# Optimization experiments

Hardware: AMD Instinct MI355X
Metric: run time of the kernel (lower is better)

Reference implementation:

```python
import jax, jax.numpy as jnp
import numpy as np
from jax import lax

B, CIN, H, W = 64, 3, 64, 64
HID = 128          # hidden_dim == embedding_dim
K = 1024           # num_embeddings
BETA = 0.25        # commitment cost


def _conv(x, w, b, stride):
    # torch Conv2d, padding=0, NCHW / OIHW weights
    y = lax.conv_general_dilated(x, w, (stride, stride), 'VALID',
                                 dimension_numbers=('NCHW', 'OIHW', 'NCHW'))
    return y + b[None, :, None, None]


def _conv_transpose(x, w, b, stride):
    # torch ConvTranspose2d, padding=0; w is [Cin, Cout, kh, kw] (torch layout)
    kh, kw = w.shape[2], w.shape[3]
    w2 = jnp.flip(w, (2, 3)).transpose(1, 0, 2, 3)  # -> OIHW, spatially flipped
    y = lax.conv_general_dilated(x, w2, (1, 1),
                                 [(kh - 1, kh - 1), (kw - 1, kw - 1)],
                                 lhs_dilation=(stride, stride),
                                 dimension_numbers=('NCHW', 'OIHW', 'NCHW'))
    return y + b[None, :, None, None]


def setup_inputs() -> dict:
    key = jax.random.key(0)
    ks = jax.random.split(key, 10)
    s = 0.05
    return {
        'x':      jax.random.normal(ks[0], (B, CIN, H, W), jnp.float32),
        'enc_w1': jax.random.normal(ks[1], (HID, CIN, 4, 4), jnp.float32) * s,
        'enc_b1': jnp.zeros((HID,), jnp.float32),
        'enc_w2': jax.random.normal(ks[2], (HID, HID, 2, 2), jnp.float32) * s,
        'enc_b2': jnp.zeros((HID,), jnp.float32),
        'codebook': jax.random.uniform(ks[3], (K, HID), jnp.float32,
                                       minval=-1.0 / K, maxval=1.0 / K),
        'dec_w1': jax.random.normal(ks[4], (HID, HID, 2, 2), jnp.float32) * s,
        'dec_b1': jnp.zeros((HID,), jnp.float32),
        'dec_w2': jax.random.normal(ks[5], (HID, CIN, 4, 4), jnp.float32) * s,
        'dec_b2': jnp.zeros((CIN,), jnp.float32),
    }


def reference(x, enc_w1, enc_b1, enc_w2, enc_b2, codebook,
              dec_w1, dec_b1, dec_w2, dec_b2):
    # ---- encoder ----
    z = jax.nn.relu(_conv(x, enc_w1, enc_b1, 2))
    z = jax.nn.relu(_conv(z, enc_w2, enc_b2, 1))   # [B, HID, 30, 30]

    # ---- vector quantizer (faithful to torch reshape semantics) ----
    D = HID
    flat = z.reshape(-1, D)                        # [N, D], C-order rows
    # squared euclidean distances (argmin identical to torch.cdist argmin)
    d2 = (jnp.sum(flat * flat, axis=1, keepdims=True)
          - 2.0 * flat @ codebook.T
          + jnp.sum(codebook * codebook, axis=1)[None, :])  # [N, K]
    idx = jnp.argmin(d2, axis=1)                   # [N]
    quantized = codebook[idx].reshape(z.shape)

    e_latent = jnp.mean((lax.stop_gradient(quantized) - z) ** 2)
    q_latent = jnp.mean((quantized - lax.stop_gradient(z)) ** 2)
    loss = q_latent + BETA * e_latent

    q_st = z + lax.stop_gradient(quantized - z)    # straight-through

    n = flat.shape[0]
    avg_probs = jnp.zeros((K,), z.dtype).at[idx].add(1.0) / n
    perplexity = jnp.exp(-jnp.sum(avg_probs * jnp.log(avg_probs + 1e-10)))

    # ---- decoder ----
    y = jax.nn.relu(_conv_transpose(q_st, dec_w1, dec_b1, 1))
    x_recon = _conv_transpose(y, dec_w2, dec_b2, 2)  # [B, 3, 64, 64]
    return x_recon, loss, perplexity
```

## Files before the change

### kernel.cpp

```cpp
#include <hip/hip_runtime.h>

#define B_    64
#define CIN_  3
#define HW_   64
#define HID_  128
#define K_    1024
#define H1_   31
#define H2_   30
#define NROWS_ 57600
#define NELEM_ 7372800

typedef __bf16 bf16_t;
typedef __attribute__((ext_vector_type(8))) __bf16 bf16x8;
typedef __attribute__((ext_vector_type(4))) float f32x4;

__global__ __launch_bounds__(256) void wprep_k(const float* __restrict__ ew1,
    const float* __restrict__ ew2, const float* __restrict__ dw1,
    const float* __restrict__ dw2, const float* __restrict__ cb,
    bf16_t* __restrict__ wc1, bf16_t* __restrict__ wc2,
    bf16_t* __restrict__ wd1, bf16_t* __restrict__ wt2,
    bf16_t* __restrict__ cbb, float* __restrict__ cnorm,
    unsigned* __restrict__ hist, float* __restrict__ sse) {
  int id = blockIdx.x * 256 + threadIdx.x;
  int t = id >> 14, co = (id >> 7) & 127, ci = id & 127;
  wc2[id] = (bf16_t)ew2[(co * 128 + ci) * 4 + t];
  wd1[id] = (bf16_t)dw1[(ci * 128 + co) * 4 + (3 - t)];
  if (id < 8192) {
    int n = id >> 9, k = id & 511;
    int tap = k >> 7, c = k & 127;
    if (n < 12) {
      int nco = n >> 2, ph = (n >> 1) & 1, pw = n & 1;
      int off = (tap >> 1) * 8 + (tap & 1) * 2;
      wt2[id] = (bf16_t)dw2[c * 48 + nco * 16 + ph * 4 + pw + off];
    } else {
      wt2[id] = (bf16_t)0.f;
    }
    int c1 = id >> 6, k1 = id & 63;
    wc1[id] = (bf16_t)(k1 < 48 ? ew1[c1 * 48 + k1] : 0.f);
  }
  if (id < K_) {
    float s0 = 0.f;
    for (int d = 0; d < HID_; d += 4) {
      float4 v = *(const float4*)&cb[id * HID_ + d];
      bf16_t tt[4] = {(bf16_t)v.x, (bf16_t)v.y, (bf16_t)v.z, (bf16_t)v.w};
      *(ushort4*)&((ushort*)cbb)[id * HID_ + d] = *(ushort4*)tt;
      float f0 = (float)tt[0], f1 = (float)tt[1];
      float f2 = (float)tt[2], f3 = (float)tt[3];
      s0 += f0 * f0 + f1 * f1 + f2 * f2 + f3 * f3;
    }
    cnorm[id] = s0;
    hist[id] = 0u;
  }
  if (id == 0) *sse = 0.f;
}

__global__ __launch_bounds__(256, 2) void conv1m_k(const float* __restrict__ x,
    const bf16_t* __restrict__ wc1, const float* __restrict__ bias,
    ushort* __restrict__ z1t) {
  __shared__ __align__(16) bf16_t as_[64 * 72];
  __shared__ __align__(16) bf16_t bs_[128 * 72];
  int b = blockIdx.x >> 4, rt = blockIdx.x & 15;
  int tid = threadIdx.x, wv = tid >> 6, ln = tid & 63;
  const float* xb = x + (size_t)b * 12288;
  #pragma unroll
  for (int it = 0; it < 16; ++it) {
    int e = it * 256 + tid;
    int p = e >> 6, k = e & 63;
    float v = 0.f;
    if (k < 48) {
      int ci = k >> 4, kh = (k >> 2) & 3, kw = k & 3;
      int row = 2 * rt + (p >> 5); if (row > 30) row = 30;
      int col = p & 31;            if (col > 30) col = 30;
      v = xb[ci * 4096 + (2 * row + kh) * 64 + 2 * col + kw];
    }
    as_[p * 72 + k] = (bf16_t)v;
  }
  {
    const float4* wg = (const float4*)wc1;
    #pragma unroll
    for (int it = 0; it < 4; ++it) {
      int fi = it * 256 + tid;
      int co = fi >> 3, k8 = fi & 7;
      *(float4*)&bs_[co * 72 + k8 * 8] = wg[fi];
    }
  }
  __syncthreads();
  int q = ln >> 4, l = ln & 15;
  f32x4 acc8[8];
  #pragma unroll
  for (int c = 0; c < 8; ++c) acc8[c] = (f32x4){0.f, 0.f, 0.f, 0.f};
  bf16x8 af[2];
  #pragma unroll
  for (int kk = 0; kk < 2; ++kk)
    af[kk] = *(const bf16x8*)&as_[(wv * 16 + l) * 72 + kk * 32 + q * 8];
  #pragma unroll
  for (int cot = 0; cot < 8; ++cot) {
    #pragma unroll
    for (int kk = 0; kk < 2; ++kk) {
      bf16x8 bf = *(const bf16x8*)&bs_[(cot * 16 + l) * 72 + kk * 32 + q * 8];
      acc8[cot] = __builtin_amdgcn_mfma_f32_16x16x32_bf16(af[kk], bf,
                                                          acc8[cot], 0, 0, 0);
    }
  }
  #pragma unroll
  for (int cot = 0; cot < 8; ++cot) {
    int co = cot * 16 + l;
    float bv = bias[co];
    #pragma unroll
    for (int r = 0; r < 4; ++r) {
      int pos = wv * 16 + q * 4 + r;
      int prow = 2 * rt + (pos >> 5), pcol = pos & 31;
      if (prow < 31 && pcol < 31) {
        float v = fmaxf(acc8[cot][r] + bv, 0.f);
        bf16_t h = (bf16_t)v;
        z1t[((size_t)(b * 1024 + prow * 32 + pcol)) * 128 + co] = *(ushort*)&h;
      }
    }
  }
}

__global__ __launch_bounds__(256, 2) void conv2m_k(const bf16_t* __restrict__ z1t,
    const bf16_t* __restrict__ wc2, const float* __restrict__ bias,
    float* __restrict__ z, ushort* __restrict__ zbuf) {
  __shared__ __align__(16) bf16_t as_[98 * 136];
  __shared__ __align__(16) bf16_t bs_[128 * 136];
  int blk = blockIdx.x;
  int b = blk / 15, rt = blk % 15;
  int tid = threadIdx.x, wv = tid >> 6, ln = tid & 63;
  const float4* src = (const float4*)(z1t + ((size_t)b * 1024 + rt * 64) * 128);
  #pragma unroll
  for (int s = 0; s < 7; ++s) {
    int f = s * 256 + tid;
    if (f < 1568) {
      int lp = f >> 4, c16 = f & 15;
      *(float4*)&as_[lp * 136 + c16 * 8] = src[f];
    }
  }
  int m = wv * 16 + (ln & 15), q = ln >> 4;
  f32x4 acc8[8];
  #pragma unroll
  for (int c = 0; c < 8; ++c) acc8[c] = (f32x4){0.f, 0.f, 0.f, 0.f};
  const float4* w4 = (const float4*)wc2;
  #pragma unroll
  for (int t = 0; t < 4; ++t) {
    __syncthreads();
    #pragma unroll
    for (int s = 0; s < 8; ++s) {
      int f = s * 256 + tid;
      int co = f >> 4, c16 = f & 15;
      *(float4*)&bs_[co * 136 + c16 * 8] = w4[t * 2048 + f];
    }
    __syncthreads();
    int off = (t >> 1) * 32 + (t & 1);
    bf16x8 af[4];
    #pragma unroll
    for (int kk = 0; kk < 4; ++kk)
      af[kk] = *(const bf16x8*)&as_[(m + off) * 136 + kk * 32 + q * 8];
    #pragma unroll
    for (int cot = 0; cot < 8; ++cot) {
      #pragma unroll
      for (int kk = 0; kk < 4; ++kk) {
        bf16x8 bf = *(const bf16x8*)&bs_[(cot * 16 + (ln & 15)) * 136 +
                                         kk * 32 + q * 8];
        acc8[cot] = __builtin_amdgcn_mfma_f32_16x16x32_bf16(af[kk], bf,
                                                            acc8[cot], 0, 0, 0);
      }
    }
  }
  #pragma unroll
  for (int cot = 0; cot < 8; ++cot) {
    int co = cot * 16 + (ln & 15);
    float bv = bias[co];
    #pragma unroll
    for (int r = 0; r < 4; ++r) {
      int mo = wv * 16 + q * 4 + r;
      int ocol = mo & 31;
      if (ocol < 30) {
        int orow = rt * 2 + (mo >> 5);
        float v = fmaxf(acc8[cot][r] + bv, 0.f);
        size_t idx = (size_t)(b * HID_ + co) * 900 + orow * 30 + ocol;
        z[idx] = v;
        bf16_t h = (bf16_t)v;
        zbuf[idx] = *(ushort*)&h;
      }
    }
  }
}

__global__ __launch_bounds__(256) void zero_k(float4* __restrict__ p, int n4) {
  int i = blockIdx.x * 256 + threadIdx.x;
  if (i < n4) p[i] = make_float4(0.f, 0.f, 0.f, 0.f);
}

__global__ __launch_bounds__(256, 2) void vq1_k(const bf16_t* __restrict__ zb,
    const bf16_t* __restrict__ cbb, const float* __restrict__ cnorm,
    int* __restrict__ idxArr, unsigned* __restrict__ hist) {
  __shared__ __align__(16) bf16_t zs[64 * 136];
  __shared__ __align__(16) bf16_t cbs[128 * 136];
  __shared__ unsigned long long red[64 * 16];
  __shared__ float cns[K_];
  int n0 = blockIdx.x * 64;
  int tid = threadIdx.x;
  int wv = tid >> 6, ln = tid & 63;
  {
    const float4* zg4 = (const float4*)(zb + (size_t)n0 * HID_);
    #pragma unroll
    for (int s = 0; s < 4; ++s) {
      int f = s * 256 + tid;
      int row = f >> 4, seg = f & 15;
      *(float4*)&zs[row * 136 + seg * 8] = zg4[f];
    }
    ((float4*)cns)[tid] = ((const float4*)cnorm)[tid];
  }
  __syncthreads();
  bf16x8 afr[4];
  #pragma unroll
  for (int kk = 0; kk < 4; ++kk)
    afr[kk] = *(const bf16x8*)&zs[(wv * 16 + (ln & 15)) * 136 + kk * 32 +
                                  (ln >> 4) * 8];
  unsigned long long best[4] = {~0ull, ~0ull, ~0ull, ~0ull};
  const float4* cg4 = (const float4*)cbb;
  for (int c0 = 0; c0 < K_; c0 += 128) {
    __syncthreads();
    #pragma unroll
    for (int s = 0; s < 8; ++s) {
      int f = s * 256 + tid;
      int code = f >> 4, seg = f & 15;
      *(float4*)&cbs[code * 136 + seg * 8] = cg4[(c0 + code) * 16 + seg];
    }
    __syncthreads();
    #pragma unroll 2
    for (int t = 0; t < 8; ++t) {
      f32x4 acc = {0.f, 0.f, 0.f, 0.f};
      #pragma unroll
      for (int kk = 0; kk < 4; ++kk) {
        bf16x8 bfr = *(const bf16x8*)&cbs[(t * 16 + (ln & 15)) * 136 +
                                          kk * 32 + (ln >> 4) * 8];
        acc = __builtin_amdgcn_mfma_f32_16x16x32_bf16(afr[kk], bfr, acc,
                                                      0, 0, 0);
      }
      int code = c0 + t * 16 + (ln & 15);
      float cn = cns[code];
      #pragma unroll
      for (int r = 0; r < 4; ++r) {
        float dist = cn - 2.f * acc[r];
        unsigned u = __float_as_uint(dist);
        u = (u & 0x80000000u) ? ~u : (u | 0x80000000u);
        unsigned long long p = ((unsigned long long)u << 32) | (unsigned)code;
        if (p < best[r]) best[r] = p;
      }
    }
  }
  __syncthreads();
  #pragma unroll
  for (int r = 0; r < 4; ++r)
    red[(wv * 16 + (ln >> 4) * 4 + r) * 16 + (ln & 15)] = best[r];
  __syncthreads();
  if (tid < 64) {
    unsigned long long b = ~0ull;
    #pragma unroll
    for (int c = 0; c < 16; ++c) {
      unsigned long long p = red[tid * 16 + c];
      if (p < b) b = p;
    }
    int bi = (int)(b & 0xffffffffu);
    idxArr[n0 + tid] = bi;
    atomicAdd(&hist[bi], 1u);
  }
}

__global__ __launch_bounds__(256) void tq_k(const bf16_t* __restrict__ cbb,
    const int* __restrict__ idxArr, ushort* __restrict__ qt) {
  __shared__ ushort t[60 * 128];
  int b = blockIdx.x / 15, st = blockIdx.x % 15;
  int tid = threadIdx.x;
  int s0 = st * 60;
  #pragma unroll
  for (int it = 0; it < 8; ++it) {
    int task = it * 256 + tid;
    if (task < 1920) {
      int sc = task >> 7, c = task & 127;
      int f = b * 115200 + c * 900 + s0 + sc * 4;
      int n = f >> 7, d = f & 127;
      int k = idxArr[n];
      ushort4 v = *(const ushort4*)((const ushort*)cbb + k * 128 + d);
      t[(sc * 4 + 0) * 128 + c] = v.x;
      t[(sc * 4 + 1) * 128 + c] = v.y;
      t[(sc * 4 + 2) * 128 + c] = v.z;
      t[(sc * 4 + 3) * 128 + c] = v.w;
    }
  }
  __syncthreads();
  #pragma unroll
  for (int it = 0; it < 4; ++it) {
    int task = it * 256 + tid;
    if (task < 960) {
      int sl = task >> 4, c16 = task & 15;
      int s = s0 + sl;
      int h = s / 30, w = s - h * 30;
      int p = (h + 1) * 32 + (w + 1);
      *(uint4*)&qt[((size_t)(b * 1024 + p)) * 128 + c16 * 8] =
          *(uint4*)&t[sl * 128 + c16 * 8];
    }
  }
}

__global__ __launch_bounds__(256) void sse_k(const float4* __restrict__ z4,
    const float* __restrict__ cb, const int* __restrict__ idxArr,
    float* __restrict__ sse) {
  int base = blockIdx.x * 2048 + threadIdx.x;
  float se = 0.f;
  #pragma unroll
  for (int it = 0; it < 8; ++it) {
    int i = base + it * 256;
    int f = i * 4;
    int n = f >> 7, d = f & 127;
    int k = idxArr[n];
    float4 zv = z4[i];
    float4 cv = *(const float4*)&cb[k * 128 + d];
    float dx = cv.x - zv.x, dy = cv.y - zv.y;
    float dz = cv.z - zv.z, dw = cv.w - zv.w;
    se += dx * dx + dy * dy + dz * dz + dw * dw;
  }
  #pragma unroll
  for (int o = 32; o > 0; o >>= 1) se += __shfl_down(se, o, 64);
  __shared__ float red[4];
  if ((threadIdx.x & 63) == 0) red[threadIdx.x >> 6] = se;
  __syncthreads();
  if (threadIdx.x == 0)
    atomicAdd(sse, red[0] + red[1] + red[2] + red[3]);
}

__global__ __launch_bounds__(256, 2) void convt1m_k(const bf16_t* __restrict__ qt,
    const bf16_t* __restrict__ wd1, const float* __restrict__ bias,
    ushort* __restrict__ yt) {
  __shared__ __align__(16) bf16_t as_[98 * 136];
  __shared__ __align__(16) bf16_t bs_[128 * 136];
  int blk = blockIdx.x;
  int b = blk >> 4, rt = blk & 15;
  int tid = threadIdx.x, wv = tid >> 6, ln = tid & 63;
  const float4* src = (const float4*)(qt + (size_t)b * 1024 * 128);
  #pragma unroll
  for (int s = 0; s < 7; ++s) {
    int f = s * 256 + tid;
    if (f < 1568) {
      int lp = f >> 4, c16 = f & 15;
      int gr = rt * 64 + lp;
      if (gr > 1023) gr = 1023;
      *(float4*)&as_[lp * 136 + c16 * 8] = src[gr * 16 + c16];
    }
  }
  int m = wv * 16 + (ln & 15), q = ln >> 4;
  f32x4 acc8[8];
  #pragma unroll
  for (int c = 0; c < 8; ++c) acc8[c] = (f32x4){0.f, 0.f, 0.f, 0.f};
  const float4* w4 = (const float4*)wd1;
  #pragma unroll
  for (int t = 0; t < 4; ++t) {
    __syncthreads();
    #pragma unroll
    for (int s = 0; s < 8; ++s) {
      int f = s * 256 + tid;
      int co = f >> 4, c16 = f & 15;
      *(float4*)&bs_[co * 136 + c16 * 8] = w4[t * 2048 + f];
    }
    __syncthreads();
    int off = (t >> 1) * 32 + (t & 1);
    bf16x8 af[4];
    #pragma unroll
    for (int kk = 0; kk < 4; ++kk)
      af[kk] = *(const bf16x8*)&as_[(m + off) * 136 + kk * 32 + q * 8];
    #pragma unroll
    for (int cot = 0; cot < 8; ++cot) {
      #pragma unroll
      for (int kk = 0; kk < 4; ++kk) {
        bf16x8 bf = *(const bf16x8*)&bs_[(cot * 16 + (ln & 15)) * 136 +
                                         kk * 32 + q * 8];
        acc8[cot] = __builtin_amdgcn_mfma_f32_16x16x32_bf16(af[kk], bf,
                                                            acc8[cot], 0, 0, 0);
      }
    }
  }
  #pragma unroll
  for (int cot = 0; cot < 8; ++cot) {
    int co = cot * 16 + (ln & 15);
    float bv = bias[co];
    #pragma unroll
    for (int r = 0; r < 4; ++r) {
      int mo = wv * 16 + q * 4 + r;
      int orow = rt * 2 + (mo >> 5), ocol = mo & 31;
      if (orow < 31 && ocol < 31) {
        float v = fmaxf(acc8[cot][r] + bv, 0.f);
        bf16_t h = (bf16_t)v;
        yt[((size_t)b * 1156 + (orow + 1) * 34 + (ocol + 1)) * 128 + co] =
            *(ushort*)&h;
      }
    }
  }
}

__global__ __launch_bounds__(256, 2) void convt2m_k(const bf16_t* __restrict__ yt,
    const bf16_t* __restrict__ wt2, const float* __restrict__ bias,
    float* __restrict__ out) {
  __shared__ __align__(16) bf16_t as_[128 * 136];
  int b = blockIdx.x >> 4, rt = blockIdx.x & 15;
  int tid = threadIdx.x, wv = tid >> 6, ln = tid & 63;
  const float4* src = (const float4*)(yt + ((size_t)b * 1156 + rt * 68) * 128);
  #pragma unroll
  for (int s = 0; s < 8; ++s) {
    int f = s * 256 + tid;
    int lp = f >> 4, c16 = f & 15;
    *(float4*)&as_[lp * 136 + c16 * 8] = src[f];
  }
  __syncthreads();
  int mloc = wv * 16 + (ln & 15), q = ln >> 4;
  int qh = mloc >> 5, qw = mloc & 31;
  int base = (qh + 1) * 34 + qw + 1;
  f32x4 acc = {0.f, 0.f, 0.f, 0.f};
  #pragma unroll
  for (int kc = 0; kc < 16; ++kc) {
    int tap = kc >> 2;
    int toff = (tap & 1) + (tap >> 1) * 34;
    bf16x8 af = *(const bf16x8*)&as_[(base - toff) * 136 +
                                     (kc & 3) * 32 + q * 8];
    bf16x8 bf = *(const bf16x8*)&wt2[(size_t)(ln & 15) * 512 + kc * 32 + q * 8];
    acc = __builtin_amdgcn_mfma_f32_16x16x32_bf16(af, bf, acc, 0, 0, 0);
  }
  __syncthreads();
  float* bb = (float*)as_;
  #pragma unroll
  for (int r = 0; r < 4; ++r)
    bb[(wv * 16 + q * 4 + r) * 16 + (ln & 15)] = acc[r];
  __syncthreads();
  if (tid < 192) {
    int row_id = tid >> 4;
    int co = row_id >> 2, ohoff = row_id & 3;
    int qhl = ohoff >> 1, ph = ohoff & 1;
    float bv = bias[co];
    int ow0 = (tid & 15) * 4;
    float tmp[4];
    #pragma unroll
    for (int e = 0; e < 4; ++e) {
      int ow = ow0 + e;
      tmp[e] = bb[(qhl * 32 + (ow >> 1)) * 16 + co * 4 + ph * 2 + (ow & 1)]
               + bv;
    }
    *(float4*)&out[((size_t)(b * 3 + co)) * 4096 + (rt * 4 + ohoff) * 64 + ow0]
        = *(float4*)tmp;
  }
}

__global__ __launch_bounds__(256) void fin_k(const unsigned* __restrict__ hist,
    const float* __restrict__ sse, float* __restrict__ out) {
  __shared__ float red[256];
  float e = 0.f;
  for (int k = threadIdx.x; k < K_; k += 256) {
    float p = (float)hist[k] * (1.0f / (float)NROWS_);
    e += p * logf(p + 1e-10f);
  }
  red[threadIdx.x] = e;
  __syncthreads();
  #pragma unroll
  for (int t = 128; t > 0; t >>= 1) {
    if (threadIdx.x < t) red[threadIdx.x] += red[threadIdx.x + t];
    __syncthreads();
  }
  if (threadIdx.x == 0) {
    out[786432] = 1.25f * (*sse) * (1.0f / (float)NELEM_);
    out[786433] = expf(-red[0]);
  }
}

extern "C" void kernel_launch(void* const* d_in, const int* in_sizes, int n_in,
                              void* d_out, int out_size, void* d_ws,
                              size_t ws_size, hipStream_t stream) {
  (void)in_sizes; (void)n_in; (void)out_size; (void)ws_size;
  const float* x   = (const float*)d_in[0];
  const float* ew1 = (const float*)d_in[1];
  const float* eb1 = (const float*)d_in[2];
  const float* ew2 = (const float*)d_in[3];
  const float* eb2 = (const float*)d_in[4];
  const float* cb  = (const float*)d_in[5];
  const float* dw1 = (const float*)d_in[6];
  const float* db1 = (const float*)d_in[7];
  const float* dw2 = (const float*)d_in[8];
  const float* db2 = (const float*)d_in[9];
  float* out = (float*)d_out;
  char* ws = (char*)d_ws;

  ushort*   yt    = (ushort*)(ws);
  float*    z     = (float*)(ws + 35684352);
  bf16_t*   z1t   = (bf16_t*)(ws + 65175552);
  bf16_t*   qt    = (bf16_t*)(ws + 65175552);
  ushort*   zbuf  = (ushort*)(ws + 81985536);
  bf16_t*   cbb   = (bf16_t*)(ws + 96731136);
  bf16_t*   wc2   = (bf16_t*)(ws + 96993280);
  bf16_t*   wd1   = (bf16_t*)(ws + 97124352);
  int*      idxArr= (int*)(ws + 97255424);
  unsigned* hist  = (unsigned*)(ws + 97485824);
  float*    cnorm = (float*)(ws + 97489920);
  float*    sse   = (float*)(ws + 97494016);
  bf16_t*   wt2   = (bf16_t*)(ws + 97497088);
  bf16_t*   wc1   = (bf16_t*)(ws + 97513472);

  wprep_k<<<dim3(256), dim3(256), 0, stream>>>(ew1, ew2, dw1, dw2, cb,
                                               wc1, wc2, wd1, wt2,
                                               cbb, cnorm, hist, sse);
  conv1m_k<<<dim3(1024), dim3(256), 0, stream>>>(x, wc1, eb1, (ushort*)z1t);
  conv2m_k<<<dim3(960), dim3(256), 0, stream>>>(z1t, wc2, eb2, z, zbuf);
  vq1_k<<<dim3(900), dim3(256), 0, stream>>>((const bf16_t*)zbuf, cbb, cnorm,
                                             idxArr, hist);
  zero_k<<<dim3(4624), dim3(256), 0, stream>>>((float4*)yt, 1183744);
  zero_k<<<dim3(4104), dim3(256), 0, stream>>>((float4*)qt, 1050624);
  tq_k<<<dim3(960), dim3(256), 0, stream>>>(cbb, idxArr, (ushort*)qt);
  sse_k<<<dim3(900), dim3(256), 0, stream>>>((const float4*)z, cb, idxArr,
                                             sse);
  convt1m_k<<<dim3(1024), dim3(256), 0, stream>>>(qt, wd1, db1, yt);
  convt2m_k<<<dim3(1024), dim3(256), 0, stream>>>((const bf16_t*)yt, wt2, db2,
                                                  out);
  fin_k<<<dim3(1), dim3(256), 0, stream>>>(hist, sse, out);
}
```

Measured before the change: 270.8 us.

## Zero only padding halos, fuse gather/SSE kernels, fold finalize into decoder

Removes the two full-buffer zeroing passes over the padded qt and yt activation buffers. Only the halo border cells are now zeroed: qt's borders in extra blocks of a new fused gather+SSE kernel, and yt's borders inside convt1m before its interior writes. The codebook gather/transpose and the SSE reduction are merged into one launch by splitting on block index, and the perplexity/loss finalize is folded into block 0 of convt2m. This cuts tens of MB of memory writes and several kernel launches. In exchange the border-index logic must exactly match the padding layout, and block 0 of convt2m does extra work.

```diff
diff --git a/kernel.cpp b/kernel.cpp
--- a/kernel.cpp
+++ b/kernel.cpp
@@ -187,11 +187,6 @@
   }
 }
 
-__global__ __launch_bounds__(256) void zero_k(float4* __restrict__ p, int n4) {
-  int i = blockIdx.x * 256 + threadIdx.x;
-  if (i < n4) p[i] = make_float4(0.f, 0.f, 0.f, 0.f);
-}
-
 __global__ __launch_bounds__(256, 2) void vq1_k(const bf16_t* __restrict__ zb,
     const bf16_t* __restrict__ cbb, const float* __restrict__ cnorm,
     int* __restrict__ idxArr, unsigned* __restrict__ hist) {
@@ -269,66 +264,82 @@
   }
 }
 
-__global__ __launch_bounds__(256) void tq_k(const bf16_t* __restrict__ cbb,
-    const int* __restrict__ idxArr, ushort* __restrict__ qt) {
+__global__ __launch_bounds__(256) void tqsse_k(const float4* __restrict__ z4,
+    const float* __restrict__ cb, const bf16_t* __restrict__ cbb,
+    const int* __restrict__ idxArr, ushort* __restrict__ qt,
+    float* __restrict__ sse) {
   __shared__ ushort t[60 * 128];
-  int b = blockIdx.x / 15, st = blockIdx.x % 15;
-  int tid = threadIdx.x;
-  int s0 = st * 60;
-  #pragma unroll
-  for (int it = 0; it < 8; ++it) {
-    int task = it * 256 + tid;
-    if (task < 1920) {
-      int sc = task >> 7, c = task & 127;
-      int f = b * 115200 + c * 900 + s0 + sc * 4;
+  __shared__ float red4[4];
+  int bid = blockIdx.x, tid = threadIdx.x;
+  if (bid < 900) {
+    int base = bid * 2048 + tid;
+    float se = 0.f;
+    #pragma unroll
+    for (int it = 0; it < 8; ++it) {
+      int i = base + it * 256;
+      int f = i * 4;
       int n = f >> 7, d = f & 127;
       int k = idxArr[n];
-      ushort4 v = *(const ushort4*)((const ushort*)cbb + k * 128 + d);
-      t[(sc * 4 + 0) * 128 + c] = v.x;
-      t[(sc * 4 + 1) * 128 + c] = v.y;
-      t[(sc * 4 + 2) * 128 + c] = v.z;
-      t[(sc * 4 + 3) * 128 + c] = v.w;
-    }
-  }
-  __syncthreads();
-  #pragma unroll
-  for (int it = 0; it < 4; ++it) {
-    int task = it * 256 + tid;
-    if (task < 960) {
-      int sl = task >> 4, c16 = task & 15;
-      int s = s0 + sl;
-      int h = s / 30, w = s - h * 30;
-      int p = (h + 1) * 32 + (w + 1);
-      *(uint4*)&qt[((size_t)(b * 1024 + p)) * 128 + c16 * 8] =
-          *(uint4*)&t[sl * 128 + c16 * 8];
-    }
-  }
-}
-
-__global__ __launch_bounds__(256) void sse_k(const float4* __restrict__ z4,
-    const float* __restrict__ cb, const int* __restrict__ idxArr,
-    float* __restrict__ sse) {
-  int base = blockIdx.x * 2048 + threadIdx.x;
-  float se = 0.f;
-  #pragma unroll
-  for (int it = 0; it < 8; ++it) {
-    int i = base + it * 256;
-    int f = i * 4;
-    int n = f >> 7, d = f & 127;
-    int k = idxArr[n];
-    float4 zv = z4[i];
-    float4 cv = *(const float4*)&cb[k * 128 + d];
-    float dx = cv.x - zv.x, dy = cv.y - zv.y;
-    float dz = cv.z - zv.z, dw = cv.w - zv.w;
-    se += dx * dx + dy * dy + dz * dz + dw * dw;
-  }
-  #pragma unroll
-  for (int o = 32; o > 0; o >>= 1) se += __shfl_down(se, o, 64);
-  __shared__ float red[4];
-  if ((threadIdx.x & 63) == 0) red[threadIdx.x >> 6] = se;
-  __syncthreads();
-  if (threadIdx.x == 0)
-    atomicAdd(sse, red[0] + red[1] + red[2] + red[3]);
+      float4 zv = z4[i];
+      float4 cv = *(const float4*)&cb[k * 128 + d];
+      float dx = cv.x - zv.x, dy = cv.y - zv.y;
+      float dz = cv.z - zv.z, dw = cv.w - zv.w;
+      se += dx * dx + dy * dy + dz * dz + dw * dw;
+    }
+    #pragma unroll
+    for (int o = 32; o > 0; o >>= 1) se += __shfl_down(se, o, 64);
+    if ((tid & 63) == 0) red4[tid >> 6] = se;
+    __syncthreads();
+    if (tid == 0) atomicAdd(sse, red4[0] + red4[1] + red4[2] + red4[3]);
+  } else if (bid < 1860) {
+    int tb = bid - 900;
+    int b = tb / 15, st = tb % 15;
+    int s0 = st * 60;
+    #pragma unroll
+    for (int it = 0; it < 8; ++it) {
+      int task = it * 256 + tid;
+      if (task < 1920) {
+        int sc = task >> 7, c = task & 127;
+        int f = b * 115200 + c * 900 + s0 + sc * 4;
+        int n = f >> 7, d = f & 127;
+        int k = idxArr[n];
+        ushort4 v = *(const ushort4*)((const ushort*)cbb + k * 128 + d);
+        t[(sc * 4 + 0) * 128 + c] = v.x;
+        t[(sc * 4 + 1) * 128 + c] = v.y;
+        t[(sc * 4 + 2) * 128 + c] = v.z;
+        t[(sc * 4 + 3) * 128 + c] = v.w;
+      }
+    }
+    __syncthreads();
+    #pragma unroll
+    for (int it = 0; it < 4; ++it) {
+      int task = it * 256 + tid;
+      if (task < 960) {
+        int sl = task >> 4, c16 = task & 15;
+        int s = s0 + sl;
+        int h = s / 30, w = s - h * 30;
+        int p = (h + 1) * 32 + (w + 1);
+        *(uint4*)&qt[((size_t)(b * 1024 + p)) * 128 + c16 * 8] =
+            *(uint4*)&t[sl * 128 + c16 * 8];
+      }
+    }
+  } else {
+    int zb_ = (bid - 1860) * 4;
+    uint4 zz = {0u, 0u, 0u, 0u};
+    for (int e = tid; e < 4 * 124 * 16; e += 256) {
+      int bb = zb_ + e / (124 * 16);
+      int rem = e % (124 * 16);
+      int pe = rem >> 4, s16 = rem & 15;
+      int p;
+      if (pe < 32) p = pe;
+      else if (pe < 64) p = 31 * 32 + (pe - 32);
+      else {
+        int idx = pe - 64;
+        p = (1 + (idx >> 1)) * 32 + ((idx & 1) ? 31 : 0);
+      }
+      *(uint4*)&qt[((size_t)(bb * 1024 + p)) * 128 + s16 * 8] = zz;
+    }
+  }
 }
 
 __global__ __launch_bounds__(256, 2) void convt1m_k(const bf16_t* __restrict__ qt,
@@ -339,6 +350,26 @@
   int blk = blockIdx.x;
   int b = blk >> 4, rt = blk & 15;
   int tid = threadIdx.x, wv = tid >> 6, ln = tid & 63;
+  {
+    uint4 zz = {0u, 0u, 0u, 0u};
+    ushort* ytb = yt + (size_t)b * 1156 * 128;
+    int nrows = (rt < 15) ? 2 : 1;
+    int r0 = 2 * rt + 1;
+    for (int e = tid; e < nrows * 48; e += 256) {
+      int rr = e / 48, rem = e % 48, cc = rem / 16, s16 = rem % 16;
+      int col = (cc == 0) ? 0 : (cc == 1 ? 32 : 33);
+      *(uint4*)&ytb[((size_t)((r0 + rr) * 34 + col)) * 128 + s16 * 8] = zz;
+    }
+    if (rt == 0)
+      for (int e = tid; e < 34 * 16; e += 256)
+        *(uint4*)&ytb[((size_t)(e >> 4)) * 128 + (e & 15) * 8] = zz;
+    if (rt == 15)
+      for (int e = tid; e < 2 * 34 * 16; e += 256) {
+        int rr = 32 + e / 544, rem = e % 544;
+        *(uint4*)&ytb[((size_t)(rr * 34 + (rem >> 4))) * 128 + (rem & 15) * 8]
+            = zz;
+      }
+  }
   const float4* src = (const float4*)(qt + (size_t)b * 1024 * 128);
   #pragma unroll
   for (int s = 0; s < 7; ++s) {
@@ -401,8 +432,10 @@
 
 __global__ __launch_bounds__(256, 2) void convt2m_k(const bf16_t* __restrict__ yt,
     const bf16_t* __restrict__ wt2, const float* __restrict__ bias,
+    const unsigned* __restrict__ hist, const float* __restrict__ sse,
     float* __restrict__ out) {
   __shared__ __align__(16) bf16_t as_[128 * 136];
+  __shared__ float redf[256];
   int b = blockIdx.x >> 4, rt = blockIdx.x & 15;
   int tid = threadIdx.x, wv = tid >> 6, ln = tid & 63;
   const float4* src = (const float4*)(yt + ((size_t)b * 1156 + rt * 68) * 128);
@@ -448,26 +481,23 @@
     *(float4*)&out[((size_t)(b * 3 + co)) * 4096 + (rt * 4 + ohoff) * 64 + ow0]
         = *(float4*)tmp;
   }
-}
-
-__global__ __launch_bounds__(256) void fin_k(const unsigned* __restrict__ hist,
-    const float* __restrict__ sse, float* __restrict__ out) {
-  __shared__ float red[256];
-  float e = 0.f;
-  for (int k = threadIdx.x; k < K_; k += 256) {
-    float p = (float)hist[k] * (1.0f / (float)NROWS_);
-    e += p * logf(p + 1e-10f);
-  }
-  red[threadIdx.x] = e;
-  __syncthreads();
-  #pragma unroll
-  for (int t = 128; t > 0; t >>= 1) {
-    if (threadIdx.x < t) red[threadIdx.x] += red[threadIdx.x + t];
-    __syncthreads();
-  }
-  if (threadIdx.x == 0) {
-    out[786432] = 1.25f * (*sse) * (1.0f / (float)NELEM_);
-    out[786433] = expf(-red[0]);
+  if (blockIdx.x == 0) {
+    float e = 0.f;
+    for (int k = tid; k < K_; k += 256) {
+      float p = (float)hist[k] * (1.0f / (float)NROWS_);
+      e += p * logf(p + 1e-10f);
+    }
+    redf[tid] = e;
+    __syncthreads();
+    #pragma unroll
+    for (int t = 128; t > 0; t >>= 1) {
+      if (tid < t) redf[tid] += redf[tid + t];
+      __syncthreads();
+    }
+    if (tid == 0) {
+      out[786432] = 1.25f * (*sse) * (1.0f / (float)NELEM_);
+      out[786433] = expf(-redf[0]);
+    }
   }
 }
 
@@ -510,13 +540,9 @@
   conv2m_k<<<dim3(960), dim3(256), 0, stream>>>(z1t, wc2, eb2, z, zbuf);
   vq1_k<<<dim3(900), dim3(256), 0, stream>>>((const bf16_t*)zbuf, cbb, cnorm,
                                              idxArr, hist);
-  zero_k<<<dim3(4624), dim3(256), 0, stream>>>((float4*)yt, 1183744);
-  zero_k<<<dim3(4104), dim3(256), 0, stream>>>((float4*)qt, 1050624);
-  tq_k<<<dim3(960), dim3(256), 0, stream>>>(cbb, idxArr, (ushort*)qt);
-  sse_k<<<dim3(900), dim3(256), 0, stream>>>((const float4*)z, cb, idxArr,
-                                             sse);
+  tqsse_k<<<dim3(1876), dim3(256), 0, stream>>>((const float4*)z, cb, cbb,
+                                                idxArr, (ushort*)qt, sse);
   convt1m_k<<<dim3(1024), dim3(256), 0, stream>>>(qt, wd1, db1, yt);
   convt2m_k<<<dim3(1024), dim3(256), 0, stream>>>((const bf16_t*)yt, wt2, db2,
-                                                  out);
-  fin_k<<<dim3(1), dim3(256), 0, stream>>>(hist, sse, out);
-}
+                                                  hist, sse, out);
+}
```

Measured after the change: 254.6 us. -6.0%, faster.
